# Optimization experiments

Measured on AMD Instinct MI355X. Metric: run time of the kernel, lower is better.

The kernel has to match this reference:

```python
import jax, jax.numpy as jnp
import numpy as np

NAT, NN = 10000, 32
RSN, THETAN, NEMB = 16, 8, 4
RC = 5.0
ZETA = 16.0
FEAT = RSN * NEMB + RSN * THETAN * NEMB  # 576
PI = 3.141592653589793


def setup_inputs() -> dict:
    key = jax.random.key(0)
    ks = jax.random.split(key, 12)
    positions = jax.random.normal(ks[0], (NAT, 3), dtype=jnp.float32) * 2.0
    species_encoder = jax.random.normal(ks[1], (NAT, NEMB), dtype=jnp.float32)
    theta_s = jax.random.uniform(ks[2], (THETAN,), dtype=jnp.float32) * PI
    kn_rad = jnp.ones((1,), dtype=jnp.float32)
    neighbor_idx = jax.random.randint(ks[3], (NAT, NN), 0, NAT, dtype=jnp.int32)
    W1 = jax.random.normal(ks[4], (FEAT, 64), dtype=jnp.float32) / np.sqrt(FEAT)
    b1 = jnp.zeros((64,), dtype=jnp.float32)
    W2 = jax.random.normal(ks[5], (64, 64), dtype=jnp.float32) / 8.0
    b2 = jnp.zeros((64,), dtype=jnp.float32)
    W3 = jax.random.normal(ks[6], (64, 1), dtype=jnp.float32) / 8.0
    b3 = jnp.zeros((1,), dtype=jnp.float32)
    return {"positions": positions, "species_encoder": species_encoder,
            "theta_s": theta_s, "kn_rad": kn_rad,
            "W1": W1, "b1": b1, "W2": W2, "b2": b2, "W3": W3, "b3": b3,
            "neighbor_idx": neighbor_idx}


def _bessel_radial(rnorm, kn_rad):
    # spherical-Bessel radial basis with smooth cosine cutoff (help_fn.bessel_function)
    fc = 0.5 * (jnp.cos(PI * rnorm / RC) + 1.0) * (rnorm < RC).astype(rnorm.dtype)
    k = jnp.arange(1, RSN + 1, dtype=rnorm.dtype)                     # [RSN]
    arg = (PI / RC) * kn_rad[0] * k[None, None, :] * rnorm[..., None]  # [nat,NN,RSN]
    return jnp.sqrt(2.0 / RC) * jnp.sin(arg) / rnorm[..., None] * fc[..., None]


def reference(positions, species_encoder, theta_s, kn_rad,
              W1, b1, W2, b2, W3, b3, neighbor_idx):
    # gather neighbor displacements: [nat, NN, 3]
    rij = positions[neighbor_idx] - positions[:, None, :]
    rnorm = jnp.linalg.norm(rij, axis=-1) + 1e-8                      # [nat, NN]

    bf = _bessel_radial(rnorm, kn_rad)                                # [nat, NN, RSN]
    # center-x-neighbor species embedding product (einsum 'ijk->ik->ijk')
    semb_ij = species_encoder[neighbor_idx] * species_encoder[:, None, :]  # [nat,NN,NEMB]

    # radial descriptors: [nat, RSN, NEMB] -> [nat, RSN*NEMB]
    desc_rad = jnp.einsum('ijl,ijm->ilm', bf, semb_ij).reshape(NAT, -1)

    # angular part
    rij_unit = rij / rnorm[..., None]
    cos_ijk = jnp.einsum('ijc,ikc->ijk', rij_unit, rij_unit)          # [nat,NN,NN]
    cos_ijk = jnp.clip(cos_ijk, -1.0 + 1e-6, 1.0 - 1e-6)
    sin_ijk = jnp.sqrt(1.0 - cos_ijk * cos_ijk)
    ct, st = jnp.cos(theta_s), jnp.sin(theta_s)

    # factorized per-bond channel tensor P: [nat, NN, RSN*NEMB]
    P = jnp.einsum('ijl,ijm->ijlm', bf, semb_ij).reshape(NAT, NN, RSN * NEMB)
    pref = 2.0 ** (1.0 - ZETA)
    ang = []
    for t in range(THETAN):  # small fixed loop over angle centers
        cosd = cos_ijk * ct[t] + sin_ijk * st[t]                      # cos(theta - theta_s)
        A = pref * (1.0 + cosd) ** ZETA                               # [nat,NN,NN]
        C = jnp.einsum('ijk,ijp->ikp', A, P)                          # contract over j
        ang.append(jnp.sum(C * P, axis=1))                            # [nat, RSN*NEMB]
    desc_ang = jnp.stack(ang, axis=1).reshape(NAT, -1)                # [nat, THETAN*RSN*NEMB]

    desc = jnp.concatenate([desc_rad, desc_ang], axis=1)              # [nat, FEAT]

    # per-atom MLP -> atomic energies, scatter-sum to total energy
    h = jnp.tanh(desc @ W1 + b1)
    h = jnp.tanh(h @ W2 + b2)
    e_atom = (h @ W3 + b3)[:, 0]                                      # [nat]
    return jnp.sum(e_atom)
```

## Files before the change

### kernel.cpp

```cpp
#include <hip/hip_runtime.h>
#include <hip/hip_bf16.h>

#define NATC 10000
#define NATP 10016
#define NNC 32
#define RSNC 16
#define THETANC 8
#define NEMBC 4
#define FEATC 576

typedef __attribute__((ext_vector_type(8))) short short8;
typedef __attribute__((ext_vector_type(4))) float f32x4;

static __device__ __forceinline__ short f2bf(float x) {
    union { __hip_bfloat16 h; short s; } u;
    u.h = __float2bfloat16(x);
    return u.s;
}

__global__ __launch_bounds__(256) void prep_kernel(
    const float* __restrict__ W1, const float* __restrict__ W2,
    ushort* __restrict__ W1p, ushort* __restrict__ W2p)
{
    const int gid = blockIdx.x * 256 + threadIdx.x;
    if (gid < 4608) {
        const int l = gid & 63, ntks = gid >> 6;
        const int nt = ntks & 3, ks = ntks >> 2;
        const int q = l >> 4, c = l & 15;
        ushort pk[8];
        #pragma unroll
        for (int jj = 0; jj < 8; ++jj)
            pk[jj] = (ushort)f2bf(W1[(ks * 32 + q * 8 + jj) * 64 + nt * 16 + c]);
        #pragma unroll
        for (int jj = 0; jj < 8; ++jj) W1p[gid * 8 + jj] = pk[jj];
    } else {
        const int g = gid - 4608;
        const int l = g & 63, ntks = g >> 6;
        const int nt = ntks & 3, ks = ntks >> 2;
        const int q = l >> 4, c = l & 15;
        ushort pk[8];
        #pragma unroll
        for (int jj = 0; jj < 8; ++jj)
            pk[jj] = (ushort)f2bf(W2[(ks * 32 + q * 8 + jj) * 64 + nt * 16 + c]);
        #pragma unroll
        for (int jj = 0; jj < 8; ++jj) W2p[g * 8 + jj] = pk[jj];
    }
}

__global__ __launch_bounds__(256, 4) void desc_kernel(
    const float* __restrict__ pos,
    const float* __restrict__ spe,
    const float* __restrict__ theta_s,
    const float* __restrict__ kn_rad,
    const int* __restrict__ nidx,
    ushort* __restrict__ descb)
{
    constexpr float RC = 5.0f;
    constexpr float PI_F = 3.14159265358979323846f;
    constexpr float PREF = 3.0517578125e-05f;

    __shared__ __attribute__((aligned(16))) float ux[NNC], uy[NNC], uz[NNC];
    __shared__ __attribute__((aligned(16))) float rbase[NNC], rw[NNC];
    __shared__ __attribute__((aligned(16))) float bfs[NNC * 17];
    __shared__ __attribute__((aligned(16))) float ses[NNC * 5];
    __shared__ __attribute__((aligned(16))) float P[NNC * 65];
    __shared__ __attribute__((aligned(16))) float cosm[NNC * 33];
    __shared__ __attribute__((aligned(16))) float sinm[NNC * 33];
    __shared__ __attribute__((aligned(16))) short Pb[4 * 64 * 8];

    const int i   = blockIdx.x;
    const int tid = threadIdx.x;

    if (tid < NNC) {
        const int j = tid;
        const int n = nidx[i * NNC + j];
        const float pix = pos[i * 3 + 0], piy = pos[i * 3 + 1], piz = pos[i * 3 + 2];
        const float dx = pos[n * 3 + 0] - pix;
        const float dy = pos[n * 3 + 1] - piy;
        const float dz = pos[n * 3 + 2] - piz;
        const float r = sqrtf(dx * dx + dy * dy + dz * dz) + 1e-8f;
        const float inv = 1.0f / r;
        ux[j] = dx * inv; uy[j] = dy * inv; uz[j] = dz * inv;
        const float fc = (r < RC) ? 0.5f * (cosf(PI_F * r * (1.0f / RC)) + 1.0f) : 0.0f;
        rbase[j] = sqrtf(2.0f / RC) * inv * fc;
        rw[j]    = (PI_F / RC) * kn_rad[0] * r;
        #pragma unroll
        for (int m = 0; m < NEMBC; ++m)
            ses[j * 5 + m] = spe[n * NEMBC + m] * spe[i * NEMBC + m];
    }
    __syncthreads();

    #pragma unroll
    for (int k = 0; k < 2; ++k) {
        const int e = tid + k * 256;
        const int j = e >> 4, l = e & 15;
        bfs[j * 17 + l] = rbase[j] * sinf(rw[j] * (float)(l + 1));
    }
    __syncthreads();

    #pragma unroll
    for (int k = 0; k < 8; ++k) {
        const int e = tid + k * 256;
        const int j = e >> 6, p = e & 63;
        P[j * 65 + p] = bfs[j * 17 + (p >> 2)] * ses[j * 5 + (p & 3)];
    }
    #pragma unroll
    for (int k = 0; k < 4; ++k) {
        const int idx = tid + k * 256;
        const int j = idx >> 5, kk = idx & 31;
        float c = ux[j] * ux[kk] + uy[j] * uy[kk] + uz[j] * uz[kk];
        c = fminf(fmaxf(c, -1.0f + 1e-6f), 1.0f - 1e-6f);
        cosm[j * 33 + kk] = c;
        sinm[j * 33 + kk] = sqrtf(fmaxf(1.0f - c * c, 0.0f));
    }
    __syncthreads();

    {
        const int nt = tid >> 6, l2 = tid & 63;
        const int q2 = l2 >> 4, c2 = l2 & 15;
        short8 pk;
        #pragma unroll
        for (int jj = 0; jj < 8; ++jj)
            pk[jj] = f2bf(P[(q2 * 8 + jj) * 65 + nt * 16 + c2]);
        *(short8*)&Pb[(nt * 64 + l2) * 8] = pk;
    }
    if (tid < 64) {
        float s = 0.0f;
        #pragma unroll 8
        for (int j = 0; j < NNC; ++j) s += P[j * 65 + tid];
        descb[(size_t)i * FEATC + tid] = (ushort)f2bf(s);
    }
    __syncthreads();

    const int w = tid >> 6, l = tid & 63;
    const int q = l >> 4, c = l & 15;

    for (int tt = 0; tt < 2; ++tt) {
        const int t = w + tt * 4;
        const float th = theta_s[t];
        const float ct = cosf(th), st = sinf(th);

        short8 afr[2];
        #pragma unroll
        for (int mt = 0; mt < 2; ++mt) {
            const int kk = mt * 16 + c;
            #pragma unroll
            for (int jj = 0; jj < 8; ++jj) {
                const int j = q * 8 + jj;
                const float cv = cosm[kk * 33 + j];
                const float sv = sinm[kk * 33 + j];
                const float cosd = fmaf(cv, ct, sv * st);
                const float x = 1.0f + cosd;
                const float x2 = x * x, x4 = x2 * x2, x8 = x4 * x4;
                afr[mt][jj] = f2bf(PREF * (x8 * x8));
            }
        }

        f32x4 acc[2][4];
        #pragma unroll
        for (int mt = 0; mt < 2; ++mt)
            #pragma unroll
            for (int nt = 0; nt < 4; ++nt)
                acc[mt][nt] = (f32x4){0.0f, 0.0f, 0.0f, 0.0f};

        #pragma unroll
        for (int nt = 0; nt < 4; ++nt) {
            const short8 bfr = *(const short8*)&Pb[(nt * 64 + l) * 8];
            acc[0][nt] = __builtin_amdgcn_mfma_f32_16x16x32_bf16(afr[0], bfr, acc[0][nt], 0, 0, 0);
            acc[1][nt] = __builtin_amdgcn_mfma_f32_16x16x32_bf16(afr[1], bfr, acc[1][nt], 0, 0, 0);
        }

        float pt[4];
        #pragma unroll
        for (int nt = 0; nt < 4; ++nt) {
            float s = 0.0f;
            #pragma unroll
            for (int mt = 0; mt < 2; ++mt)
                #pragma unroll
                for (int r = 0; r < 4; ++r) {
                    const int kk = mt * 16 + q * 4 + r;
                    s = fmaf(acc[mt][nt][r], P[kk * 65 + nt * 16 + c], s);
                }
            s += __shfl_xor(s, 16, 64);
            s += __shfl_xor(s, 32, 64);
            pt[nt] = s;
        }
        const float v = (q == 0) ? pt[0] : (q == 1) ? pt[1] : (q == 2) ? pt[2] : pt[3];
        descb[(size_t)i * FEATC + 64 + t * 64 + l] = (ushort)f2bf(v);
    }
}

__global__ __launch_bounds__(256) void mlp_kernel(
    const ushort* __restrict__ descb,
    const ushort* __restrict__ W1p, const float* __restrict__ b1,
    const ushort* __restrict__ W2p, const float* __restrict__ b2,
    const float* __restrict__ W3, const float* __restrict__ b3,
    float* __restrict__ out)
{
    __shared__ __attribute__((aligned(16))) ushort H1b[32 * 72];
    __shared__ float red[4];

    const int tid = threadIdx.x;
    const int w = tid >> 6, l = tid & 63;
    const int q = l >> 4, c = l & 15;
    const int a0 = blockIdx.x * 32;

    f32x4 acc[2];
    acc[0] = (f32x4){0.0f, 0.0f, 0.0f, 0.0f};
    acc[1] = (f32x4){0.0f, 0.0f, 0.0f, 0.0f};

    #pragma unroll 3
    for (int ks = 0; ks < 18; ++ks) {
        const short8 b = *(const short8*)&W1p[((ks * 4 + w) * 64 + l) * 8];
        #pragma unroll
        for (int mt = 0; mt < 2; ++mt) {
            const int a = a0 + mt * 16 + c;
            const short8 afr = *(const short8*)&descb[(size_t)a * FEATC + ks * 32 + q * 8];
            acc[mt] = __builtin_amdgcn_mfma_f32_16x16x32_bf16(afr, b, acc[mt], 0, 0, 0);
        }
    }

    const float b1v = b1[w * 16 + c];
    #pragma unroll
    for (int mt = 0; mt < 2; ++mt)
        #pragma unroll
        for (int r = 0; r < 4; ++r) {
            const int m = mt * 16 + q * 4 + r;
            H1b[m * 72 + w * 16 + c] = (ushort)f2bf(tanhf(acc[mt][r] + b1v));
        }
    __syncthreads();

    f32x4 acc2[2];
    acc2[0] = (f32x4){0.0f, 0.0f, 0.0f, 0.0f};
    acc2[1] = (f32x4){0.0f, 0.0f, 0.0f, 0.0f};
    #pragma unroll
    for (int ks = 0; ks < 2; ++ks) {
        const short8 b = *(const short8*)&W2p[((ks * 4 + w) * 64 + l) * 8];
        #pragma unroll
        for (int mt = 0; mt < 2; ++mt) {
            const short8 afr = *(const short8*)&H1b[(mt * 16 + c) * 72 + ks * 32 + q * 8];
            acc2[mt] = __builtin_amdgcn_mfma_f32_16x16x32_bf16(afr, b, acc2[mt], 0, 0, 0);
        }
    }

    const float b2v = b2[w * 16 + c];
    const float w3v = W3[w * 16 + c];
    float s = 0.0f;
    #pragma unroll
    for (int mt = 0; mt < 2; ++mt)
        #pragma unroll
        for (int r = 0; r < 4; ++r) {
            const int a = a0 + mt * 16 + q * 4 + r;
            const float e = tanhf(acc2[mt][r] + b2v) * w3v;
            if (a < NATC) s += e;
        }
    #pragma unroll
    for (int off = 1; off <= 32; off <<= 1)
        s += __shfl_xor(s, off, 64);
    if (l == 0) red[w] = s;
    __syncthreads();
    if (tid == 0) {
        float tot = red[0] + red[1] + red[2] + red[3];
        if (blockIdx.x == 0) tot += (float)NATC * b3[0];
        atomicAdd(out, tot);
    }
}

extern "C" void kernel_launch(void* const* d_in, const int* in_sizes, int n_in,
                              void* d_out, int out_size, void* d_ws, size_t ws_size,
                              hipStream_t stream)
{
    const float* pos   = (const float*)d_in[0];
    const float* spe   = (const float*)d_in[1];
    const float* theta = (const float*)d_in[2];
    const float* kn    = (const float*)d_in[3];
    const float* W1    = (const float*)d_in[4];
    const float* b1    = (const float*)d_in[5];
    const float* W2    = (const float*)d_in[6];
    const float* b2    = (const float*)d_in[7];
    const float* W3    = (const float*)d_in[8];
    const float* b3    = (const float*)d_in[9];
    const int*   nidx  = (const int*)d_in[10];
    float* out = (float*)d_out;

    ushort* descb = (ushort*)d_ws;
    ushort* W1p   = (ushort*)((char*)d_ws + (size_t)NATP * FEATC * 2);
    ushort* W2p   = W1p + 4608 * 8;

    hipMemsetAsync(out, 0, sizeof(float), stream);
    prep_kernel<<<20, 256, 0, stream>>>(W1, W2, W1p, W2p);
    desc_kernel<<<NATC, 256, 0, stream>>>(pos, spe, theta, kn, nidx, descb);
    mlp_kernel<<<(NATC + 31) / 32, 256, 0, stream>>>(descb, W1p, b1, W2p, b2, W3, b3, out);
}
```

Before: 154.3 us.

## Fuse per-atom MLP into descriptor kernel and reduce energies deterministically

The per-atom MLP now runs at the end of the descriptor kernel on a shared-memory descriptor row, so the bf16 descriptor matrix is never written to or read back from global memory. The first layer uses an MFMA with only one live row, wasting most of the matrix unit. The second layer runs as scalar FMAs in one wave, reading W2 from global memory. A single-block reduce kernel replaces the atomics and the memset, and the P row stride changes from 65 to 66. This trades a separate MLP pass with good MFMA use for a serial per-block tail that adds latency to every atom's block.

```diff
diff --git a/kernel.cpp b/kernel.cpp
--- a/kernel.cpp
+++ b/kernel.cpp
@@ -2,7 +2,6 @@
 #include <hip/hip_bf16.h>
 
 #define NATC 10000
-#define NATP 10016
 #define NNC 32
 #define RSNC 16
 #define THETANC 8
@@ -19,32 +18,18 @@
 }
 
 __global__ __launch_bounds__(256) void prep_kernel(
-    const float* __restrict__ W1, const float* __restrict__ W2,
-    ushort* __restrict__ W1p, ushort* __restrict__ W2p)
+    const float* __restrict__ W1, ushort* __restrict__ W1p)
 {
     const int gid = blockIdx.x * 256 + threadIdx.x;
-    if (gid < 4608) {
-        const int l = gid & 63, ntks = gid >> 6;
-        const int nt = ntks & 3, ks = ntks >> 2;
-        const int q = l >> 4, c = l & 15;
-        ushort pk[8];
-        #pragma unroll
-        for (int jj = 0; jj < 8; ++jj)
-            pk[jj] = (ushort)f2bf(W1[(ks * 32 + q * 8 + jj) * 64 + nt * 16 + c]);
-        #pragma unroll
-        for (int jj = 0; jj < 8; ++jj) W1p[gid * 8 + jj] = pk[jj];
-    } else {
-        const int g = gid - 4608;
-        const int l = g & 63, ntks = g >> 6;
-        const int nt = ntks & 3, ks = ntks >> 2;
-        const int q = l >> 4, c = l & 15;
-        ushort pk[8];
-        #pragma unroll
-        for (int jj = 0; jj < 8; ++jj)
-            pk[jj] = (ushort)f2bf(W2[(ks * 32 + q * 8 + jj) * 64 + nt * 16 + c]);
-        #pragma unroll
-        for (int jj = 0; jj < 8; ++jj) W2p[g * 8 + jj] = pk[jj];
-    }
+    const int l = gid & 63, ntks = gid >> 6;
+    const int nt = ntks & 3, ks = ntks >> 2;
+    const int q = l >> 4, c = l & 15;
+    ushort pk[8];
+    #pragma unroll
+    for (int jj = 0; jj < 8; ++jj)
+        pk[jj] = (ushort)f2bf(W1[(ks * 32 + q * 8 + jj) * 64 + nt * 16 + c]);
+    #pragma unroll
+    for (int jj = 0; jj < 8; ++jj) W1p[gid * 8 + jj] = pk[jj];
 }
 
 __global__ __launch_bounds__(256, 4) void desc_kernel(
@@ -53,7 +38,13 @@
     const float* __restrict__ theta_s,
     const float* __restrict__ kn_rad,
     const int* __restrict__ nidx,
-    ushort* __restrict__ descb)
+    const ushort* __restrict__ W1p,
+    const float* __restrict__ b1,
+    const float* __restrict__ W2,
+    const float* __restrict__ b2,
+    const float* __restrict__ W3,
+    const float* __restrict__ b3,
+    float* __restrict__ e_atom)
 {
     constexpr float RC = 5.0f;
     constexpr float PI_F = 3.14159265358979323846f;
@@ -63,10 +54,13 @@
     __shared__ __attribute__((aligned(16))) float rbase[NNC], rw[NNC];
     __shared__ __attribute__((aligned(16))) float bfs[NNC * 17];
     __shared__ __attribute__((aligned(16))) float ses[NNC * 5];
-    __shared__ __attribute__((aligned(16))) float P[NNC * 65];
+    __shared__ __attribute__((aligned(16))) float P[NNC * 66];
     __shared__ __attribute__((aligned(16))) float cosm[NNC * 33];
     __shared__ __attribute__((aligned(16))) float sinm[NNC * 33];
     __shared__ __attribute__((aligned(16))) short Pb[4 * 64 * 8];
+    __shared__ __attribute__((aligned(16))) ushort drow[FEATC];
+    __shared__ __attribute__((aligned(16))) float h1p[64];
+    __shared__ __attribute__((aligned(16))) float h1f[64];
 
     const int i   = blockIdx.x;
     const int tid = threadIdx.x;
@@ -102,7 +96,7 @@
     for (int k = 0; k < 8; ++k) {
         const int e = tid + k * 256;
         const int j = e >> 6, p = e & 63;
-        P[j * 65 + p] = bfs[j * 17 + (p >> 2)] * ses[j * 5 + (p & 3)];
+        P[j * 66 + p] = bfs[j * 17 + (p >> 2)] * ses[j * 5 + (p & 3)];
     }
     #pragma unroll
     for (int k = 0; k < 4; ++k) {
@@ -121,14 +115,14 @@
         short8 pk;
         #pragma unroll
         for (int jj = 0; jj < 8; ++jj)
-            pk[jj] = f2bf(P[(q2 * 8 + jj) * 65 + nt * 16 + c2]);
+            pk[jj] = f2bf(P[(q2 * 8 + jj) * 66 + nt * 16 + c2]);
         *(short8*)&Pb[(nt * 64 + l2) * 8] = pk;
     }
     if (tid < 64) {
         float s = 0.0f;
         #pragma unroll 8
-        for (int j = 0; j < NNC; ++j) s += P[j * 65 + tid];
-        descb[(size_t)i * FEATC + tid] = (ushort)f2bf(s);
+        for (int j = 0; j < NNC; ++j) s += P[j * 66 + tid];
+        drow[tid] = (ushort)f2bf(s);
     }
     __syncthreads();
 
@@ -179,91 +173,61 @@
                 #pragma unroll
                 for (int r = 0; r < 4; ++r) {
                     const int kk = mt * 16 + q * 4 + r;
-                    s = fmaf(acc[mt][nt][r], P[kk * 65 + nt * 16 + c], s);
+                    s = fmaf(acc[mt][nt][r], P[kk * 66 + nt * 16 + c], s);
                 }
             s += __shfl_xor(s, 16, 64);
             s += __shfl_xor(s, 32, 64);
             pt[nt] = s;
         }
         const float v = (q == 0) ? pt[0] : (q == 1) ? pt[1] : (q == 2) ? pt[2] : pt[3];
-        descb[(size_t)i * FEATC + 64 + t * 64 + l] = (ushort)f2bf(v);
-    }
-}
-
-__global__ __launch_bounds__(256) void mlp_kernel(
-    const ushort* __restrict__ descb,
-    const ushort* __restrict__ W1p, const float* __restrict__ b1,
-    const ushort* __restrict__ W2p, const float* __restrict__ b2,
-    const float* __restrict__ W3, const float* __restrict__ b3,
-    float* __restrict__ out)
-{
-    __shared__ __attribute__((aligned(16))) ushort H1b[32 * 72];
+        drow[64 + t * 64 + l] = (ushort)f2bf(v);
+    }
+    __syncthreads();
+
+    {
+        f32x4 acc1 = (f32x4){0.0f, 0.0f, 0.0f, 0.0f};
+        const short8 zero8 = (short8){0, 0, 0, 0, 0, 0, 0, 0};
+        #pragma unroll 3
+        for (int ks = 0; ks < 18; ++ks) {
+            const short8 bfr = *(const short8*)&W1p[((ks * 4 + w) * 64 + l) * 8];
+            short8 afr = *(const short8*)&drow[ks * 32 + q * 8];
+            if (c != 0) afr = zero8;
+            acc1 = __builtin_amdgcn_mfma_f32_16x16x32_bf16(afr, bfr, acc1, 0, 0, 0);
+        }
+        if (l < 16) h1p[w * 16 + l] = acc1[0];
+    }
+    __syncthreads();
+
+    if (tid < 64) {
+        h1f[tid] = tanhf(h1p[tid] + b1[tid]);
+        float acc2 = b2[tid];
+        #pragma unroll 8
+        for (int k = 0; k < 64; ++k)
+            acc2 = fmaf(h1f[k], W2[k * 64 + tid], acc2);
+        float s = tanhf(acc2) * W3[tid];
+        #pragma unroll
+        for (int off = 1; off <= 32; off <<= 1)
+            s += __shfl_xor(s, off, 64);
+        if (tid == 0) e_atom[i] = s + b3[0];
+    }
+}
+
+__global__ __launch_bounds__(256) void reduce_kernel(
+    const float* __restrict__ e_atom, float* __restrict__ out)
+{
     __shared__ float red[4];
-
     const int tid = threadIdx.x;
-    const int w = tid >> 6, l = tid & 63;
-    const int q = l >> 4, c = l & 15;
-    const int a0 = blockIdx.x * 32;
-
-    f32x4 acc[2];
-    acc[0] = (f32x4){0.0f, 0.0f, 0.0f, 0.0f};
-    acc[1] = (f32x4){0.0f, 0.0f, 0.0f, 0.0f};
-
-    #pragma unroll 3
-    for (int ks = 0; ks < 18; ++ks) {
-        const short8 b = *(const short8*)&W1p[((ks * 4 + w) * 64 + l) * 8];
-        #pragma unroll
-        for (int mt = 0; mt < 2; ++mt) {
-            const int a = a0 + mt * 16 + c;
-            const short8 afr = *(const short8*)&descb[(size_t)a * FEATC + ks * 32 + q * 8];
-            acc[mt] = __builtin_amdgcn_mfma_f32_16x16x32_bf16(afr, b, acc[mt], 0, 0, 0);
-        }
-    }
-
-    const float b1v = b1[w * 16 + c];
-    #pragma unroll
-    for (int mt = 0; mt < 2; ++mt)
-        #pragma unroll
-        for (int r = 0; r < 4; ++r) {
-            const int m = mt * 16 + q * 4 + r;
-            H1b[m * 72 + w * 16 + c] = (ushort)f2bf(tanhf(acc[mt][r] + b1v));
-        }
-    __syncthreads();
-
-    f32x4 acc2[2];
-    acc2[0] = (f32x4){0.0f, 0.0f, 0.0f, 0.0f};
-    acc2[1] = (f32x4){0.0f, 0.0f, 0.0f, 0.0f};
-    #pragma unroll
-    for (int ks = 0; ks < 2; ++ks) {
-        const short8 b = *(const short8*)&W2p[((ks * 4 + w) * 64 + l) * 8];
-        #pragma unroll
-        for (int mt = 0; mt < 2; ++mt) {
-            const short8 afr = *(const short8*)&H1b[(mt * 16 + c) * 72 + ks * 32 + q * 8];
-            acc2[mt] = __builtin_amdgcn_mfma_f32_16x16x32_bf16(afr, b, acc2[mt], 0, 0, 0);
-        }
-    }
-
-    const float b2v = b2[w * 16 + c];
-    const float w3v = W3[w * 16 + c];
     float s = 0.0f;
-    #pragma unroll
-    for (int mt = 0; mt < 2; ++mt)
-        #pragma unroll
-        for (int r = 0; r < 4; ++r) {
-            const int a = a0 + mt * 16 + q * 4 + r;
-            const float e = tanhf(acc2[mt][r] + b2v) * w3v;
-            if (a < NATC) s += e;
-        }
+    for (int idx = tid; idx < NATC / 4; idx += 256) {
+        const float4 v = *(const float4*)&e_atom[idx * 4];
+        s += (v.x + v.y) + (v.z + v.w);
+    }
     #pragma unroll
     for (int off = 1; off <= 32; off <<= 1)
         s += __shfl_xor(s, off, 64);
-    if (l == 0) red[w] = s;
-    __syncthreads();
-    if (tid == 0) {
-        float tot = red[0] + red[1] + red[2] + red[3];
-        if (blockIdx.x == 0) tot += (float)NATC * b3[0];
-        atomicAdd(out, tot);
-    }
+    if ((tid & 63) == 0) red[tid >> 6] = s;
+    __syncthreads();
+    if (tid == 0) out[0] = (red[0] + red[1]) + (red[2] + red[3]);
 }
 
 extern "C" void kernel_launch(void* const* d_in, const int* in_sizes, int n_in,
@@ -283,12 +247,11 @@
     const int*   nidx  = (const int*)d_in[10];
     float* out = (float*)d_out;
 
-    ushort* descb = (ushort*)d_ws;
-    ushort* W1p   = (ushort*)((char*)d_ws + (size_t)NATP * FEATC * 2);
-    ushort* W2p   = W1p + 4608 * 8;
-
-    hipMemsetAsync(out, 0, sizeof(float), stream);
-    prep_kernel<<<20, 256, 0, stream>>>(W1, W2, W1p, W2p);
-    desc_kernel<<<NATC, 256, 0, stream>>>(pos, spe, theta, kn, nidx, descb);
-    mlp_kernel<<<(NATC + 31) / 32, 256, 0, stream>>>(descb, W1p, b1, W2p, b2, W3, b3, out);
-}
+    float*  e_atom = (float*)d_ws;
+    ushort* W1p    = (ushort*)((char*)d_ws + 40000);
+
+    prep_kernel<<<18, 256, 0, stream>>>(W1, W1p);
+    desc_kernel<<<NATC, 256, 0, stream>>>(pos, spe, theta, kn, nidx,
+                                          W1p, b1, W2, b2, W3, b3, e_atom);
+    reduce_kernel<<<1, 256, 0, stream>>>(e_atom, out);
+}
```

Measured after the change: 155.0 us. About the same (+0.4%).
